# Kernel tuning notes

Hardware: AMD Instinct MI355X
Metric: run time of the kernel (lower is better)

## Reference

```python
import jax, jax.numpy as jnp
import numpy as np

DIM = 768
NUM_BLOCKS = 4
BLOCK = DIM // NUM_BLOCKS
SCALE = 0.02
LAMBDA = 0.01
EPS = 1e-5


def setup_inputs() -> dict:
    key = jax.random.key(0)
    ks = jax.random.split(key, 6)
    B, H, W = 64, 32, 32
    x = jax.random.normal(ks[0], (B, DIM, H, W), dtype=jnp.float32)
    w1 = jax.random.normal(ks[1], (2, NUM_BLOCKS, BLOCK, BLOCK), dtype=jnp.float32) * SCALE
    w2 = jax.random.normal(ks[2], (2, NUM_BLOCKS, BLOCK, BLOCK), dtype=jnp.float32) * SCALE
    b1 = jax.random.normal(ks[3], (2, NUM_BLOCKS, BLOCK), dtype=jnp.float32) * SCALE
    b2 = jax.random.normal(ks[4], (2, NUM_BLOCKS, BLOCK), dtype=jnp.float32) * SCALE
    gamma = jnp.ones((DIM,), dtype=jnp.float32)
    beta = jnp.zeros((DIM,), dtype=jnp.float32)
    return {"x": x, "w1": w1, "w2": w2, "b1": b1, "b2": b2,
            "gamma": gamma, "beta": beta, "H": H, "W": W}


def _softshrink(s, lam):
    return jnp.where(s > lam, s - lam, jnp.where(s < -lam, s + lam, jnp.zeros_like(s)))


def reference(x, w1, w2, b1, b2, gamma, beta, H, W):
    B, C = x.shape[0], x.shape[1]
    nb, bs = NUM_BLOCKS, C // NUM_BLOCKS
    # (B, C, H, W) -> (B, N, C)
    xt = x.reshape(B, C, H * W).transpose(0, 2, 1)
    residual = xt
    # LayerNorm over channel dim
    mu = jnp.mean(xt, axis=-1, keepdims=True)
    var = jnp.mean(jnp.square(xt - mu), axis=-1, keepdims=True)
    xn = (xt - mu) / jnp.sqrt(var + EPS) * gamma + beta
    # (B, N, nb, bs), FFT2 over (N, nb)
    xf = jnp.fft.fft2(xn.reshape(B, H * W, nb, bs), axes=(1, 2), norm='ortho')
    xr, xi = xf.real, xf.imag

    def mul(u, w):
        return jnp.einsum('bnqd,qdk->bnqk', u, w)  # block-diagonal matmul

    r1 = jax.nn.relu(mul(xr, w1[0]) - mul(xi, w1[1]) + b1[0])
    i1 = jax.nn.relu(mul(xr, w1[1]) + mul(xi, w1[0]) + b1[1])
    r2 = mul(r1, w2[0]) - mul(i1, w2[1]) + b2[0]
    i2 = mul(r1, w2[1]) + mul(i1, w2[0]) + b2[1]
    s = jnp.stack([r2, i2], axis=-1)
    s = _softshrink(s, LAMBDA)
    xc = jax.lax.complex(s[..., 0], s[..., 1])
    y = jnp.fft.ifft2(xc, axes=(1, 2), norm='ortho').real  # cast complex->real keeps real part
    y = y.reshape(B, H * W, C) + residual
    return y.transpose(0, 2, 1).reshape(B, C, H, W)
```

## Files before the change

kernel.cpp:

```cpp
#include <hip/hip_runtime.h>
#include <math.h>

#define BB 64
#define CC 768
#define NN 1024
#define BS 192
#define EPS 1e-5f
#define LAM 0.01f

typedef float  f32x4  __attribute__((ext_vector_type(4)));
typedef short  bf16x8 __attribute__((ext_vector_type(8)));

__device__ inline unsigned f2bf(float x) {
    unsigned u = __float_as_uint(x);
    u += 0x7fff + ((u >> 16) & 1);
    return u >> 16;
}
__device__ inline unsigned pack2(float r, float i) { return f2bf(r) | (f2bf(i) << 16); }
__device__ inline float bflo(unsigned v) { return __uint_as_float(v << 16); }
__device__ inline float bfhi(unsigned v) { return __uint_as_float(v & 0xffff0000u); }

__device__ inline int swz(int i) { return i ^ (((i >> 4) & 3) << 2); }

__global__ __launch_bounds__(512) void ln_stats(const float* __restrict__ x,
                                                float* __restrict__ mu,
                                                float* __restrict__ rstd) {
    int tn = threadIdx.x & 63, tc = threadIdx.x >> 6;
    int n = blockIdx.x * 256 + tn * 4, b = blockIdx.y;
    const float* xp = x + (size_t)b * CC * NN + n;
    f32x4 s = (f32x4)0.f, ss = (f32x4)0.f;
    #pragma unroll 4
    for (int c = tc; c < CC; c += 8) {
        f32x4 v = *(const f32x4*)(xp + (size_t)c * NN);
        s += v; ss += v * v;
    }
    __shared__ f32x4 sm[8][64], sq[8][64];
    sm[tc][tn] = s; sq[tc][tn] = ss;
    __syncthreads();
    if (tc == 0) {
        f32x4 S  = sm[0][tn], SS = sq[0][tn];
        #pragma unroll
        for (int i = 1; i < 8; i++) { S += sm[i][tn]; SS += sq[i][tn]; }
        f32x4 m = S * (1.f / 768.f);
        f32x4 r;
        #pragma unroll
        for (int i = 0; i < 4; i++) {
            float var = SS[i] * (1.f / 768.f) - m[i] * m[i];
            r[i] = rsqrtf(var + EPS);
        }
        *(f32x4*)(mu + (size_t)b * NN + n)   = m;
        *(f32x4*)(rstd + (size_t)b * NN + n) = r;
    }
}

__global__ void fwd_fft(const float* __restrict__ x,
                        const float* __restrict__ mu_, const float* __restrict__ rs_,
                        const float* __restrict__ gamma, const float* __restrict__ beta,
                        unsigned* __restrict__ Xp) {
    __shared__ float2 bufs[4][1024];
    int d = blockIdx.x, b = blockIdx.y, tid = threadIdx.x;

    float s1f, c1f;
    __sincosf(-(float)M_PI * 0.5f * (float)tid / 256.f, &s1f, &c1f);
    float c2f = c1f * c1f - s1f * s1f, s2f = 2.f * c1f * s1f;
    float c3f = c2f * c1f - s2f * s1f, s3f = c2f * s1f + s2f * c1f;

    const float* mp = mu_ + b * NN;
    const float* rp = rs_ + b * NN;
    #pragma unroll
    for (int q = 0; q < 4; q++) {
        int c = q * BS + d;
        float g = gamma[c], be = beta[c];
        const float* xp = x + ((size_t)b * CC + c) * NN;
        float v0 = (xp[tid]       - mp[tid])       * rp[tid]       * g + be;
        float v1 = (xp[tid + 256] - mp[tid + 256]) * rp[tid + 256] * g + be;
        float v2 = (xp[tid + 512] - mp[tid + 512]) * rp[tid + 512] * g + be;
        float v3 = (xp[tid + 768] - mp[tid + 768]) * rp[tid + 768] * g + be;
        float t0 = v0 + v2, t1 = v0 - v2, t2 = v1 + v3, t3 = v1 - v3;
        bufs[q][swz(tid)]       = make_float2(t0 + t2, 0.f);
        bufs[q][swz(tid + 256)] = make_float2(t1 * c1f + t3 * s1f, t1 * s1f - t3 * c1f);
        bufs[q][swz(tid + 512)] = make_float2((t0 - t2) * c2f, (t0 - t2) * s2f);
        bufs[q][swz(tid + 768)] = make_float2(t1 * c3f - t3 * s3f, t1 * s3f + t3 * c3f);
    }
    __syncthreads();

    #pragma unroll
    for (int sL = 0; sL < 3; sL++) {
        const int L = 64 >> (2 * sL);
        int j = tid & (L - 1);
        int base = ((tid - j) << 2) + j;
        float s1, c1;
        __sincosf(-(float)M_PI * 0.5f * (float)j / (float)L, &s1, &c1);
        float c2 = c1 * c1 - s1 * s1, s2 = 2.f * c1 * s1;
        float c3 = c2 * c1 - s2 * s1, s3 = c2 * s1 + s2 * c1;
        #pragma unroll
        for (int q = 0; q < 4; q++) {
            float2 a  = bufs[q][swz(base)];
            float2 bb = bufs[q][swz(base + L)];
            float2 cc = bufs[q][swz(base + 2 * L)];
            float2 dd = bufs[q][swz(base + 3 * L)];
            float t0r = a.x + cc.x, t0i = a.y + cc.y;
            float t1r = a.x - cc.x, t1i = a.y - cc.y;
            float t2r = bb.x + dd.x, t2i = bb.y + dd.y;
            float t3r = bb.x - dd.x, t3i = bb.y - dd.y;
            float X0r = t0r + t2r, X0i = t0i + t2i;
            float X2r = t0r - t2r, X2i = t0i - t2i;
            float X1r = t1r + t3i, X1i = t1i - t3r;
            float X3r = t1r - t3i, X3i = t1i + t3r;
            bufs[q][swz(base)]         = make_float2(X0r, X0i);
            bufs[q][swz(base + L)]     = make_float2(X1r * c1 - X1i * s1, X1r * s1 + X1i * c1);
            bufs[q][swz(base + 2 * L)] = make_float2(X2r * c2 - X2i * s2, X2r * s2 + X2i * c2);
            bufs[q][swz(base + 3 * L)] = make_float2(X3r * c3 - X3i * s3, X3r * s3 + X3i * c3);
        }
        __syncthreads();
    }

    float Xr[4][4], Xi[4][4];
    int i0 = swz(4 * tid);
    #pragma unroll
    for (int q = 0; q < 4; q++) {
        const float4* p = (const float4*)&bufs[q][i0];
        float4 u0 = p[0], u1 = p[1];
        float t0r = u0.x + u1.x, t0i = u0.y + u1.y;
        float t1r = u0.x - u1.x, t1i = u0.y - u1.y;
        float t2r = u0.z + u1.z, t2i = u0.w + u1.w;
        float t3r = u0.z - u1.z, t3i = u0.w - u1.w;
        Xr[q][0] = t0r + t2r; Xi[q][0] = t0i + t2i;
        Xr[q][1] = t1r + t3i; Xi[q][1] = t1i - t3r;
        Xr[q][2] = t0r - t2r; Xi[q][2] = t0i - t2i;
        Xr[q][3] = t1r - t3i; Xi[q][3] = t1i + t3r;
    }
    const float sc = 1.f / 64.f;
    unsigned o0[4], o1[4], o2[4], o3[4];
    #pragma unroll
    for (int m = 0; m < 4; m++) {
        float x0r = Xr[0][m], x0i = Xi[0][m];
        float x1r = Xr[1][m], x1i = Xi[1][m];
        float x2r = Xr[2][m], x2i = Xi[2][m];
        float x3r = Xr[3][m], x3i = Xi[3][m];
        float X0r = x0r + x1r + x2r + x3r, X0i = x0i + x1i + x2i + x3i;
        float X2r = x0r - x1r + x2r - x3r, X2i = x0i - x1i + x2i - x3i;
        float X1r = x0r + x1i - x2r - x3i, X1i = x0i - x1r - x2i + x3r;
        float X3r = x0r - x1i - x2r + x3i, X3i = x0i + x1r - x2i - x3r;
        o0[m] = pack2(X0r * sc, X0i * sc);
        o1[m] = pack2(X1r * sc, X1i * sc);
        o2[m] = pack2(X2r * sc, X2i * sc);
        o3[m] = pack2(X3r * sc, X3i * sc);
    }
    size_t qs = (size_t)BS * NN;
    size_t base = (((size_t)b * 4) * BS + d) * NN + 4 * tid;
    *(uint4*)(Xp + base)          = make_uint4(o0[0], o0[1], o0[2], o0[3]);
    *(uint4*)(Xp + base + qs)     = make_uint4(o1[0], o1[1], o1[2], o1[3]);
    *(uint4*)(Xp + base + 2 * qs) = make_uint4(o2[0], o2[1], o2[2], o2[3]);
    *(uint4*)(Xp + base + 3 * qs) = make_uint4(o3[0], o3[1], o3[2], o3[3]);
}

__global__ void pack_b(const float* __restrict__ w, unsigned* __restrict__ Bp) {
    int ch = blockIdx.x, q = blockIdx.y;
    const float* wr = w + (size_t)q * BS * BS;
    const float* wi = w + (size_t)(4 + q) * BS * BS;
    size_t base = ((size_t)q * 12 + ch) * (384 * 16);
    for (int r = 0; r < 24; r++) {
        int idx = r * 256 + threadIdx.x;
        int j = idx >> 4, dd = idx & 15;
        int h = j >> 1;
        int dg = ch * 16 + dd;
        float Wr = wr[(size_t)dg * BS + h];
        float Wi = wi[(size_t)dg * BS + h];
        Bp[base + idx] = (j & 1) ? pack2(Wi, Wr) : pack2(Wr, -Wi);
    }
}

__global__ __launch_bounds__(512, 4) void fused_mlp(const unsigned* __restrict__ Ap,
                                                    const unsigned* __restrict__ Bp1,
                                                    const unsigned* __restrict__ Bp2,
                                                    const float* __restrict__ b1,
                                                    const float* __restrict__ b2,
                                                    unsigned* __restrict__ Yp) {
    __shared__ __align__(16) unsigned tl[12288];

    const int mblk = blockIdx.x;
    const int bq   = blockIdx.y;
    const int q    = bq & 3;
    const int tid  = threadIdx.x;
    const int wave = tid >> 6;
    const int lane = tid & 63;
    const int l15  = lane & 15;
    const int quad = lane >> 4;
    const int jw   = wave * 48;

    const size_t bstride = 384 * 16;
    const unsigned* b1_lane = Bp1 + (size_t)q * 12 * bstride + (jw + l15) * 16 + quad * 4;
    const unsigned* b2_lane = Bp2 + (size_t)q * 12 * bstride + (jw + l15) * 16 + quad * 4;

    {
        const unsigned* abase = Ap + ((size_t)bq * BS) * NN + (size_t)mblk * 64;
        unsigned st[24];
        #pragma unroll
        for (int i = 0; i < 6; i++) {
            int r = (i * 8 + wave) * 4 + quad;
            const unsigned* gp = abase + (size_t)r * NN + l15;
            #pragma unroll
            for (int k = 0; k < 4; k++) st[i * 4 + k] = gp[16 * k];
        }
        #pragma unroll
        for (int i = 0; i < 6; i++) {
            int s = i * 8 + wave;
            unsigned* lp = &tl[s * 256 + quad];
            #pragma unroll
            for (int k = 0; k < 4; k++) lp[(l15 + 16 * k) * 4] = st[i * 4 + k];
        }
    }

    f32x4 acc[3][4];
    #pragma unroll
    for (int i = 0; i < 3; i++)
        #pragma unroll
        for (int j = 0; j < 4; j++)
            acc[i][j] = (f32x4)0.f;

    __syncthreads();

    #pragma unroll
    for (int ch = 0; ch < 12; ch++) {
        const unsigned* tp = &tl[(ch * 4 + quad) * 256];
        const unsigned* bp = b1_lane + ch * bstride;
        bf16x8 af[4], bfr[3];
        #pragma unroll
        for (int tn = 0; tn < 3; tn++) {
            union { uint4 u4; bf16x8 v; } bu;
            bu.u4 = *(const uint4*)(bp + tn * 256);
            bfr[tn] = bu.v;
        }
        #pragma unroll
        for (int tm = 0; tm < 4; tm++)
            af[tm] = *(const bf16x8*)(tp + (tm * 16 + l15) * 4);
        #pragma unroll
        for (int tn = 0; tn < 3; tn++)
            #pragma unroll
            for (int tm = 0; tm < 4; tm++)
                acc[tn][tm] = __builtin_amdgcn_mfma_f32_16x16x32_bf16(bfr[tn], af[tm], acc[tn][tm], 0, 0, 0);
    }

    __syncthreads();

    #pragma unroll
    for (int tn = 0; tn < 3; tn++) {
        int hg = jw >> 1;
        hg += tn * 8 + quad * 2;
        float b0r = b1[q * BS + hg];
        float b0i = b1[768 + q * BS + hg];
        float b1r_ = b1[q * BS + hg + 1];
        float b1i_ = b1[768 + q * BS + hg + 1];
        #pragma unroll
        for (int tm = 0; tm < 4; tm++) {
            int c = tm * 16 + l15;
            f32x4 a = acc[tn][tm];
            float v0 = fmaxf(a[0] + b0r, 0.f);
            float v1 = fmaxf(a[1] + b0i, 0.f);
            float v2 = fmaxf(a[2] + b1r_, 0.f);
            float v3 = fmaxf(a[3] + b1i_, 0.f);
            unsigned* hp = &tl[(hg >> 2) * 256 + c * 4 + (hg & 3)];
            *(uint2*)hp = make_uint2(pack2(v0, v1), pack2(v2, v3));
            acc[tn][tm] = (f32x4)0.f;
        }
    }
    __syncthreads();

    #pragma unroll
    for (int ch = 0; ch < 12; ch++) {
        const unsigned* tp = &tl[(ch * 4 + quad) * 256];
        const unsigned* bp = b2_lane + ch * bstride;
        bf16x8 af[4], bfr[3];
        #pragma unroll
        for (int tn = 0; tn < 3; tn++) {
            union { uint4 u4; bf16x8 v; } bu;
            bu.u4 = *(const uint4*)(bp + tn * 256);
            bfr[tn] = bu.v;
        }
        #pragma unroll
        for (int tm = 0; tm < 4; tm++)
            af[tm] = *(const bf16x8*)(tp + (tm * 16 + l15) * 4);
        #pragma unroll
        for (int tn = 0; tn < 3; tn++)
            #pragma unroll
            for (int tm = 0; tm < 4; tm++)
                acc[tn][tm] = __builtin_amdgcn_mfma_f32_16x16x32_bf16(bfr[tn], af[tm], acc[tn][tm], 0, 0, 0);
    }

    #pragma unroll
    for (int tn = 0; tn < 3; tn++) {
        int hg = (jw >> 1) + tn * 8 + quad * 2;
        float b0r = b2[q * BS + hg];
        float b0i = b2[768 + q * BS + hg];
        float b1r_ = b2[q * BS + hg + 1];
        float b1i_ = b2[768 + q * BS + hg + 1];
        size_t row0 = ((size_t)bq * BS + hg) * NN + (size_t)mblk * 64;
        #pragma unroll
        for (int tm = 0; tm < 4; tm++) {
            int mcol = tm * 16 + l15;
            f32x4 a = acc[tn][tm];
            float v0 = a[0] + b0r, v1 = a[1] + b0i;
            float v2 = a[2] + b1r_, v3 = a[3] + b1i_;
            v0 = (v0 > LAM) ? (v0 - LAM) : ((v0 < -LAM) ? (v0 + LAM) : 0.f);
            v1 = (v1 > LAM) ? (v1 - LAM) : ((v1 < -LAM) ? (v1 + LAM) : 0.f);
            v2 = (v2 > LAM) ? (v2 - LAM) : ((v2 < -LAM) ? (v2 + LAM) : 0.f);
            v3 = (v3 > LAM) ? (v3 - LAM) : ((v3 < -LAM) ? (v3 + LAM) : 0.f);
            Yp[row0 + mcol]      = pack2(v0, v1);
            Yp[row0 + NN + mcol] = pack2(v2, v3);
        }
    }
}

__global__ void inv_fft(const float* __restrict__ x,
                        const unsigned* __restrict__ Yp,
                        float* __restrict__ out) {
    __shared__ float2 bufs[4][1024];
    int d = blockIdx.x, b = blockIdx.y, tid = threadIdx.x;

    float Ar[4][4], Ai[4][4];
    size_t qs = (size_t)BS * NN;
    size_t rowb = (((size_t)b * 4) * BS + d) * NN + 4 * tid;
    #pragma unroll
    for (int q = 0; q < 4; q++) {
        uint4 v = *(const uint4*)(Yp + rowb + (size_t)q * qs);
        Ar[q][0] = bflo(v.x); Ai[q][0] = bfhi(v.x);
        Ar[q][1] = bflo(v.y); Ai[q][1] = bfhi(v.y);
        Ar[q][2] = bflo(v.z); Ai[q][2] = bfhi(v.z);
        Ar[q][3] = bflo(v.w); Ai[q][3] = bfhi(v.w);
    }
    #pragma unroll
    for (int m = 0; m < 4; m++) {
        float x0r = Ar[0][m], x0i = Ai[0][m];
        float x1r = Ar[1][m], x1i = Ai[1][m];
        float x2r = Ar[2][m], x2i = Ai[2][m];
        float x3r = Ar[3][m], x3i = Ai[3][m];
        float Y0r = x0r + x1r + x2r + x3r, Y0i = x0i + x1i + x2i + x3i;
        float Y2r = x0r - x1r + x2r - x3r, Y2i = x0i - x1i + x2i - x3i;
        float Y1r = x0r - x1i - x2r + x3i, Y1i = x0i + x1r - x2i - x3r;
        float Y3r = x0r + x1i - x2r - x3i, Y3i = x0i - x1r - x2i + x3r;
        Ar[0][m] = Y0r; Ai[0][m] = Y0i;
        Ar[1][m] = Y1r; Ai[1][m] = Y1i;
        Ar[2][m] = Y2r; Ai[2][m] = Y2i;
        Ar[3][m] = Y3r; Ai[3][m] = Y3i;
    }
    int i0 = swz(4 * tid);
    #pragma unroll
    for (int q = 0; q < 4; q++) {
        float t0r = Ar[q][0] + Ar[q][2], t0i = Ai[q][0] + Ai[q][2];
        float t1r = Ar[q][0] - Ar[q][2], t1i = Ai[q][0] - Ai[q][2];
        float t2r = Ar[q][1] + Ar[q][3], t2i = Ai[q][1] + Ai[q][3];
        float t3r = Ar[q][1] - Ar[q][3], t3i = Ai[q][1] - Ai[q][3];
        float4* p = (float4*)&bufs[q][i0];
        p[0] = make_float4(t0r + t2r, t0i + t2i, t1r - t3i, t1i + t3r);
        p[1] = make_float4(t0r - t2r, t0i - t2i, t1r + t3i, t1i - t3r);
    }
    __syncthreads();

    #pragma unroll
    for (int sL = 0; sL < 3; sL++) {
        const int L = 4 << (2 * sL);
        int j = tid & (L - 1);
        int base = ((tid - j) << 2) + j;
        float s1, c1;
        __sincosf((float)M_PI * 0.5f * (float)j / (float)L, &s1, &c1);
        float c2 = c1 * c1 - s1 * s1, s2 = 2.f * c1 * s1;
        float c3 = c2 * c1 - s2 * s1, s3 = c2 * s1 + s2 * c1;
        #pragma unroll
        for (int q = 0; q < 4; q++) {
            float2 y0 = bufs[q][swz(base)];
            float2 y1 = bufs[q][swz(base + L)];
            float2 y2 = bufs[q][swz(base + 2 * L)];
            float2 y3 = bufs[q][swz(base + 3 * L)];
            float A1r = y1.x * c1 - y1.y * s1, A1i = y1.x * s1 + y1.y * c1;
            float A2r = y2.x * c2 - y2.y * s2, A2i = y2.x * s2 + y2.y * c2;
            float A3r = y3.x * c3 - y3.y * s3, A3i = y3.x * s3 + y3.y * c3;
            float t0r = y0.x + A2r, t0i = y0.y + A2i;
            float t1r = y0.x - A2r, t1i = y0.y - A2i;
            float t2r = A1r + A3r, t2i = A1i + A3i;
            float t3r = A1r - A3r, t3i = A1i - A3i;
            bufs[q][swz(base)]         = make_float2(t0r + t2r, t0i + t2i);
            bufs[q][swz(base + L)]     = make_float2(t1r - t3i, t1i + t3r);
            bufs[q][swz(base + 2 * L)] = make_float2(t0r - t2r, t0i - t2i);
            bufs[q][swz(base + 3 * L)] = make_float2(t1r + t3i, t1i - t3r);
        }
        __syncthreads();
    }

    float s1f, c1f;
    __sincosf((float)M_PI * 0.5f * (float)tid / 256.f, &s1f, &c1f);
    float c2f = c1f * c1f - s1f * s1f, s2f = 2.f * c1f * s1f;
    float c3f = c2f * c1f - s2f * s1f, s3f = c2f * s1f + s2f * c1f;
    const float sc = 1.f / 64.f;
    #pragma unroll
    for (int q = 0; q < 4; q++) {
        float2 y0 = bufs[q][swz(tid)];
        float2 y1 = bufs[q][swz(tid + 256)];
        float2 y2 = bufs[q][swz(tid + 512)];
        float2 y3 = bufs[q][swz(tid + 768)];
        float A1r = y1.x * c1f - y1.y * s1f, A1i = y1.x * s1f + y1.y * c1f;
        float A2r = y2.x * c2f - y2.y * s2f;
        float A3r = y3.x * c3f - y3.y * s3f, A3i = y3.x * s3f + y3.y * c3f;
        float t0r = y0.x + A2r;
        float t1r = y0.x - A2r;
        float t2r = A1r + A3r;
        float t3i = A1i - A3i;
        size_t row = (((size_t)b * 4 + q) * BS + d) * NN;
        const float* xp = x + row;
        out[row + tid]       = (t0r + t2r) * sc + xp[tid];
        out[row + tid + 256] = (t1r - t3i) * sc + xp[tid + 256];
        out[row + tid + 512] = (t0r - t2r) * sc + xp[tid + 512];
        out[row + tid + 768] = (t1r + t3i) * sc + xp[tid + 768];
    }
}

extern "C" void kernel_launch(void* const* d_in, const int* in_sizes, int n_in,
                              void* d_out, int out_size, void* d_ws, size_t ws_size,
                              hipStream_t stream) {
    const float* x     = (const float*)d_in[0];
    const float* w1    = (const float*)d_in[1];
    const float* w2    = (const float*)d_in[2];
    const float* b1    = (const float*)d_in[3];
    const float* b2    = (const float*)d_in[4];
    const float* gamma = (const float*)d_in[5];
    const float* beta  = (const float*)d_in[6];

    unsigned* Xp = (unsigned*)d_ws;
    float* mu    = (float*)d_ws + (size_t)BB * CC * NN;
    float* rstd  = mu + (size_t)BB * NN;
    unsigned* Bp1 = (unsigned*)(rstd + (size_t)BB * NN);
    unsigned* Bp2 = Bp1 + (size_t)4 * 12 * 384 * 16;
    unsigned* Yp = Xp;

    pack_b<<<dim3(12, 4), 256, 0, stream>>>(w1, Bp1);
    pack_b<<<dim3(12, 4), 256, 0, stream>>>(w2, Bp2);
    ln_stats<<<dim3(NN / 256, BB), 512, 0, stream>>>(x, mu, rstd);
    fwd_fft<<<dim3(BS, BB), 256, 0, stream>>>(x, mu, rstd, gamma, beta, Xp);
    fused_mlp<<<dim3(16, 256), 512, 0, stream>>>(Xp, Bp1, Bp2, b1, b2, Yp);
    inv_fft<<<dim3(BS, BB), 256, 0, stream>>>(x, Yp, (float*)d_out);
}
```

Baseline: 705.8 us.

## Exploit real-input symmetry to halve FFT work in forward and inverse kernels

The forward FFT does the 4-point transform over blocks first and then packs the real-valued channel planes into two complex 1024-point FFTs instead of four. Hermitian symmetry recovers the separate outputs through a conjugate-index permutation (prt). The inverse kernel does the reverse packing, so only two complex inverse FFTs run, and it emits the real output from the combined planes. This halves the shared memory in the forward kernel and the LDS butterfly work, at the cost of extra shuffle passes and syncs. The MLP kernel also drops its occupancy hint and loop unrolling and reorders its fragment loads.

Result: no change. 693.2 us (median of 2 runs) (-1.8%).

```diff
diff --git a/kernel.cpp b/kernel.cpp
--- a/kernel.cpp
+++ b/kernel.cpp
@@ -21,6 +21,16 @@
 __device__ inline float bfhi(unsigned v) { return __uint_as_float(v & 0xffff0000u); }
 
 __device__ inline int swz(int i) { return i ^ (((i >> 4) & 3) << 2); }
+
+__device__ inline int rev4(int p) {
+    return ((p & 3) << 8) | ((p & 12) << 4) | (p & 48) | ((p >> 4) & 12) | ((p >> 8) & 3);
+}
+__device__ inline int prt(int p) {
+    return rev4((1024 - rev4(p)) & 1023);
+}
+__device__ inline float2 cmul(float2 z, float c, float s) {
+    return make_float2(z.x * c - z.y * s, z.x * s + z.y * c);
+}
 
 __global__ __launch_bounds__(512) void ln_stats(const float* __restrict__ x,
                                                 float* __restrict__ mu,
@@ -57,7 +67,7 @@
                         const float* __restrict__ mu_, const float* __restrict__ rs_,
                         const float* __restrict__ gamma, const float* __restrict__ beta,
                         unsigned* __restrict__ Xp) {
-    __shared__ float2 bufs[4][1024];
+    __shared__ float2 bufs[2][1024];
     int d = blockIdx.x, b = blockIdx.y, tid = threadIdx.x;
 
     float s1f, c1f;
@@ -67,20 +77,38 @@
 
     const float* mp = mu_ + b * NN;
     const float* rp = rs_ + b * NN;
+
+    float xv[4][4];
     #pragma unroll
     for (int q = 0; q < 4; q++) {
         int c = q * BS + d;
         float g = gamma[c], be = beta[c];
         const float* xp = x + ((size_t)b * CC + c) * NN;
-        float v0 = (xp[tid]       - mp[tid])       * rp[tid]       * g + be;
-        float v1 = (xp[tid + 256] - mp[tid + 256]) * rp[tid + 256] * g + be;
-        float v2 = (xp[tid + 512] - mp[tid + 512]) * rp[tid + 512] * g + be;
-        float v3 = (xp[tid + 768] - mp[tid + 768]) * rp[tid + 768] * g + be;
-        float t0 = v0 + v2, t1 = v0 - v2, t2 = v1 + v3, t3 = v1 - v3;
-        bufs[q][swz(tid)]       = make_float2(t0 + t2, 0.f);
-        bufs[q][swz(tid + 256)] = make_float2(t1 * c1f + t3 * s1f, t1 * s1f - t3 * c1f);
-        bufs[q][swz(tid + 512)] = make_float2((t0 - t2) * c2f, (t0 - t2) * s2f);
-        bufs[q][swz(tid + 768)] = make_float2(t1 * c3f - t3 * s3f, t1 * s3f + t3 * c3f);
+        #pragma unroll
+        for (int k = 0; k < 4; k++) {
+            int n = tid + 256 * k;
+            xv[q][k] = (xp[n] - mp[n]) * rp[n] * g + be;
+        }
+    }
+    float2 za[4], zb[4];
+    #pragma unroll
+    for (int k = 0; k < 4; k++) {
+        float a = xv[0][k], b1v = xv[1][k], c2v = xv[2][k], d3v = xv[3][k];
+        za[k] = make_float2(a + b1v + c2v + d3v, a - b1v + c2v - d3v);
+        zb[k] = make_float2(a - c2v, d3v - b1v);
+    }
+    #pragma unroll
+    for (int pl = 0; pl < 2; pl++) {
+        float2 z0 = pl ? zb[0] : za[0], z1 = pl ? zb[1] : za[1];
+        float2 z2 = pl ? zb[2] : za[2], z3 = pl ? zb[3] : za[3];
+        float t0r = z0.x + z2.x, t0i = z0.y + z2.y;
+        float t1r = z0.x - z2.x, t1i = z0.y - z2.y;
+        float t2r = z1.x + z3.x, t2i = z1.y + z3.y;
+        float t3r = z1.x - z3.x, t3i = z1.y - z3.y;
+        bufs[pl][swz(tid)] = make_float2(t0r + t2r, t0i + t2i);
+        bufs[pl][swz(tid + 256)] = cmul(make_float2(t1r + t3i, t1i - t3r), c1f, s1f);
+        bufs[pl][swz(tid + 512)] = cmul(make_float2(t0r - t2r, t0i - t2i), c2f, s2f);
+        bufs[pl][swz(tid + 768)] = cmul(make_float2(t1r - t3i, t1i + t3r), c3f, s3f);
     }
     __syncthreads();
 
@@ -94,11 +122,11 @@
         float c2 = c1 * c1 - s1 * s1, s2 = 2.f * c1 * s1;
         float c3 = c2 * c1 - s2 * s1, s3 = c2 * s1 + s2 * c1;
         #pragma unroll
-        for (int q = 0; q < 4; q++) {
-            float2 a  = bufs[q][swz(base)];
-            float2 bb = bufs[q][swz(base + L)];
-            float2 cc = bufs[q][swz(base + 2 * L)];
-            float2 dd = bufs[q][swz(base + 3 * L)];
+        for (int pl = 0; pl < 2; pl++) {
+            float2 a  = bufs[pl][swz(base)];
+            float2 bb = bufs[pl][swz(base + L)];
+            float2 cc = bufs[pl][swz(base + 2 * L)];
+            float2 dd = bufs[pl][swz(base + 3 * L)];
             float t0r = a.x + cc.x, t0i = a.y + cc.y;
             float t1r = a.x - cc.x, t1i = a.y - cc.y;
             float t2r = bb.x + dd.x, t2i = bb.y + dd.y;
@@ -107,45 +135,53 @@
             float X2r = t0r - t2r, X2i = t0i - t2i;
             float X1r = t1r + t3i, X1i = t1i - t3r;
             float X3r = t1r - t3i, X3i = t1i + t3r;
-            bufs[q][swz(base)]         = make_float2(X0r, X0i);
-            bufs[q][swz(base + L)]     = make_float2(X1r * c1 - X1i * s1, X1r * s1 + X1i * c1);
-            bufs[q][swz(base + 2 * L)] = make_float2(X2r * c2 - X2i * s2, X2r * s2 + X2i * c2);
-            bufs[q][swz(base + 3 * L)] = make_float2(X3r * c3 - X3i * s3, X3r * s3 + X3i * c3);
+            bufs[pl][swz(base)]         = make_float2(X0r, X0i);
+            bufs[pl][swz(base + L)]     = make_float2(X1r * c1 - X1i * s1, X1r * s1 + X1i * c1);
+            bufs[pl][swz(base + 2 * L)] = make_float2(X2r * c2 - X2i * s2, X2r * s2 + X2i * c2);
+            bufs[pl][swz(base + 3 * L)] = make_float2(X3r * c3 - X3i * s3, X3r * s3 + X3i * c3);
         }
         __syncthreads();
     }
 
-    float Xr[4][4], Xi[4][4];
     int i0 = swz(4 * tid);
-    #pragma unroll
-    for (int q = 0; q < 4; q++) {
-        const float4* p = (const float4*)&bufs[q][i0];
-        float4 u0 = p[0], u1 = p[1];
-        float t0r = u0.x + u1.x, t0i = u0.y + u1.y;
-        float t1r = u0.x - u1.x, t1i = u0.y - u1.y;
-        float t2r = u0.z + u1.z, t2i = u0.w + u1.w;
-        float t3r = u0.z - u1.z, t3i = u0.w - u1.w;
-        Xr[q][0] = t0r + t2r; Xi[q][0] = t0i + t2i;
-        Xr[q][1] = t1r + t3i; Xi[q][1] = t1i - t3r;
-        Xr[q][2] = t0r - t2r; Xi[q][2] = t0i - t2i;
-        Xr[q][3] = t1r - t3i; Xi[q][3] = t1i + t3r;
-    }
-    const float sc = 1.f / 64.f;
+    float2 A[2][4];
+    #pragma unroll
+    for (int pl = 0; pl < 2; pl++) {
+        const float4* p4 = (const float4*)&bufs[pl][i0];
+        float4 v0 = p4[0], v1 = p4[1];
+        float t0r = v0.x + v1.x, t0i = v0.y + v1.y;
+        float t1r = v0.x - v1.x, t1i = v0.y - v1.y;
+        float t2r = v0.z + v1.z, t2i = v0.w + v1.w;
+        float t3r = v0.z - v1.z, t3i = v0.w - v1.w;
+        A[pl][0] = make_float2(t0r + t2r, t0i + t2i);
+        A[pl][1] = make_float2(t1r + t3i, t1i - t3r);
+        A[pl][2] = make_float2(t0r - t2r, t0i - t2i);
+        A[pl][3] = make_float2(t1r - t3i, t1i + t3r);
+    }
+    #pragma unroll
+    for (int pl = 0; pl < 2; pl++)
+        #pragma unroll
+        for (int j = 0; j < 4; j++)
+            bufs[pl][i0 + j] = A[pl][j];
+    __syncthreads();
+
+    const float sc  = 1.f / 64.f;
+    const float sc2 = 1.f / 128.f;
     unsigned o0[4], o1[4], o2[4], o3[4];
     #pragma unroll
-    for (int m = 0; m < 4; m++) {
-        float x0r = Xr[0][m], x0i = Xi[0][m];
-        float x1r = Xr[1][m], x1i = Xi[1][m];
-        float x2r = Xr[2][m], x2i = Xi[2][m];
-        float x3r = Xr[3][m], x3i = Xi[3][m];
-        float X0r = x0r + x1r + x2r + x3r, X0i = x0i + x1i + x2i + x3i;
-        float X2r = x0r - x1r + x2r - x3r, X2i = x0i - x1i + x2i - x3i;
-        float X1r = x0r + x1i - x2r - x3i, X1i = x0i - x1r - x2i + x3r;
-        float X3r = x0r - x1i - x2r + x3i, X3i = x0i + x1r - x2i - x3r;
-        o0[m] = pack2(X0r * sc, X0i * sc);
-        o1[m] = pack2(X1r * sc, X1i * sc);
-        o2[m] = pack2(X2r * sc, X2i * sc);
-        o3[m] = pack2(X3r * sc, X3i * sc);
+    for (int j = 0; j < 4; j++) {
+        int p = 4 * tid + j;
+        int pq = prt(p);
+        float2 zap = A[0][j], zbp = A[1][j];
+        float2 zaq = bufs[0][swz(pq)];
+        float2 zbq = bufs[1][swz(pq)];
+        float p0r = zap.x + zaq.x, p0i = zap.y - zaq.y;
+        float dr  = zap.x - zaq.x, di  = zap.y + zaq.y;
+        float p2r = di, p2i = -dr;
+        o0[j] = pack2(p0r * sc2, p0i * sc2);
+        o2[j] = pack2(p2r * sc2, p2i * sc2);
+        o1[j] = pack2(zbp.x * sc, zbp.y * sc);
+        o3[j] = pack2(zbq.x * sc, -zbq.y * sc);
     }
     size_t qs = (size_t)BS * NN;
     size_t base = (((size_t)b * 4) * BS + d) * NN + 4 * tid;
@@ -171,12 +207,12 @@
     }
 }
 
-__global__ __launch_bounds__(512, 4) void fused_mlp(const unsigned* __restrict__ Ap,
-                                                    const unsigned* __restrict__ Bp1,
-                                                    const unsigned* __restrict__ Bp2,
-                                                    const float* __restrict__ b1,
-                                                    const float* __restrict__ b2,
-                                                    unsigned* __restrict__ Yp) {
+__global__ __launch_bounds__(512) void fused_mlp(const unsigned* __restrict__ Ap,
+                                                 const unsigned* __restrict__ Bp1,
+                                                 const unsigned* __restrict__ Bp2,
+                                                 const float* __restrict__ b1,
+                                                 const float* __restrict__ b2,
+                                                 unsigned* __restrict__ Yp) {
     __shared__ __align__(16) unsigned tl[12288];
 
     const int mblk = blockIdx.x;
@@ -221,21 +257,20 @@
 
     __syncthreads();
 
-    #pragma unroll
     for (int ch = 0; ch < 12; ch++) {
         const unsigned* tp = &tl[(ch * 4 + quad) * 256];
         const unsigned* bp = b1_lane + ch * bstride;
         bf16x8 af[4], bfr[3];
         #pragma unroll
+        for (int tm = 0; tm < 4; tm++)
+            af[tm] = *(const bf16x8*)(tp + (tm * 16 + l15) * 4);
+        #pragma unroll
         for (int tn = 0; tn < 3; tn++) {
             union { uint4 u4; bf16x8 v; } bu;
             bu.u4 = *(const uint4*)(bp + tn * 256);
             bfr[tn] = bu.v;
         }
         #pragma unroll
-        for (int tm = 0; tm < 4; tm++)
-            af[tm] = *(const bf16x8*)(tp + (tm * 16 + l15) * 4);
-        #pragma unroll
         for (int tn = 0; tn < 3; tn++)
             #pragma unroll
             for (int tm = 0; tm < 4; tm++)
@@ -246,8 +281,7 @@
 
     #pragma unroll
     for (int tn = 0; tn < 3; tn++) {
-        int hg = jw >> 1;
-        hg += tn * 8 + quad * 2;
+        int hg = (jw >> 1) + tn * 8 + quad * 2;
         float b0r = b1[q * BS + hg];
         float b0i = b1[768 + q * BS + hg];
         float b1r_ = b1[q * BS + hg + 1];
@@ -267,20 +301,19 @@
     }
     __syncthreads();
 
-    #pragma unroll
     for (int ch = 0; ch < 12; ch++) {
         const unsigned* tp = &tl[(ch * 4 + quad) * 256];
         const unsigned* bp = b2_lane + ch * bstride;
         bf16x8 af[4], bfr[3];
         #pragma unroll
+        for (int tm = 0; tm < 4; tm++)
+            af[tm] = *(const bf16x8*)(tp + (tm * 16 + l15) * 4);
+        #pragma unroll
         for (int tn = 0; tn < 3; tn++) {
             union { uint4 u4; bf16x8 v; } bu;
             bu.u4 = *(const uint4*)(bp + tn * 256);
             bfr[tn] = bu.v;
         }
-        #pragma unroll
-        for (int tm = 0; tm < 4; tm++)
-            af[tm] = *(const bf16x8*)(tp + (tm * 16 + l15) * 4);
         #pragma unroll
         for (int tn = 0; tn < 3; tn++)
             #pragma unroll
@@ -318,42 +351,52 @@
     __shared__ float2 bufs[4][1024];
     int d = blockIdx.x, b = blockIdx.y, tid = threadIdx.x;
 
-    float Ar[4][4], Ai[4][4];
+    float2 S[4][4];
     size_t qs = (size_t)BS * NN;
     size_t rowb = (((size_t)b * 4) * BS + d) * NN + 4 * tid;
     #pragma unroll
-    for (int q = 0; q < 4; q++) {
-        uint4 v = *(const uint4*)(Yp + rowb + (size_t)q * qs);
-        Ar[q][0] = bflo(v.x); Ai[q][0] = bfhi(v.x);
-        Ar[q][1] = bflo(v.y); Ai[q][1] = bfhi(v.y);
-        Ar[q][2] = bflo(v.z); Ai[q][2] = bfhi(v.z);
-        Ar[q][3] = bflo(v.w); Ai[q][3] = bfhi(v.w);
-    }
-    #pragma unroll
-    for (int m = 0; m < 4; m++) {
-        float x0r = Ar[0][m], x0i = Ai[0][m];
-        float x1r = Ar[1][m], x1i = Ai[1][m];
-        float x2r = Ar[2][m], x2i = Ai[2][m];
-        float x3r = Ar[3][m], x3i = Ai[3][m];
-        float Y0r = x0r + x1r + x2r + x3r, Y0i = x0i + x1i + x2i + x3i;
-        float Y2r = x0r - x1r + x2r - x3r, Y2i = x0i - x1i + x2i - x3i;
-        float Y1r = x0r - x1i - x2r + x3i, Y1i = x0i + x1r - x2i - x3r;
-        float Y3r = x0r + x1i - x2r - x3i, Y3i = x0i - x1r - x2i + x3r;
-        Ar[0][m] = Y0r; Ai[0][m] = Y0i;
-        Ar[1][m] = Y1r; Ai[1][m] = Y1i;
-        Ar[2][m] = Y2r; Ai[2][m] = Y2i;
-        Ar[3][m] = Y3r; Ai[3][m] = Y3i;
+    for (int u = 0; u < 4; u++) {
+        uint4 v = *(const uint4*)(Yp + rowb + (size_t)u * qs);
+        S[u][0] = make_float2(bflo(v.x), bfhi(v.x));
+        S[u][1] = make_float2(bflo(v.y), bfhi(v.y));
+        S[u][2] = make_float2(bflo(v.z), bfhi(v.z));
+        S[u][3] = make_float2(bflo(v.w), bfhi(v.w));
     }
     int i0 = swz(4 * tid);
     #pragma unroll
-    for (int q = 0; q < 4; q++) {
-        float t0r = Ar[q][0] + Ar[q][2], t0i = Ai[q][0] + Ai[q][2];
-        float t1r = Ar[q][0] - Ar[q][2], t1i = Ai[q][0] - Ai[q][2];
-        float t2r = Ar[q][1] + Ar[q][3], t2i = Ai[q][1] + Ai[q][3];
-        float t3r = Ar[q][1] - Ar[q][3], t3i = Ai[q][1] - Ai[q][3];
-        float4* p = (float4*)&bufs[q][i0];
-        p[0] = make_float4(t0r + t2r, t0i + t2i, t1r - t3i, t1i + t3r);
-        p[1] = make_float4(t0r - t2r, t0i - t2i, t1r + t3i, t1i - t3r);
+    for (int u = 0; u < 4; u++)
+        #pragma unroll
+        for (int j = 0; j < 4; j++)
+            bufs[u][i0 + j] = S[u][j];
+    __syncthreads();
+
+    float2 Wa[4], Wb[4];
+    #pragma unroll
+    for (int j = 0; j < 4; j++) {
+        int p = 4 * tid + j;
+        int pq = prt(p);
+        float2 s0q = bufs[0][swz(pq)];
+        float2 s2q = bufs[2][swz(pq)];
+        float2 s3q = bufs[3][swz(pq)];
+        float h0r = S[0][j].x + s0q.x, h0i = S[0][j].y - s0q.y;
+        float h2r = S[2][j].x + s2q.x, h2i = S[2][j].y - s2q.y;
+        Wa[j] = make_float2(h0r - h2i, h0i + h2r);
+        Wb[j] = make_float2(S[1][j].x + s3q.x, S[1][j].y - s3q.y);
+    }
+    __syncthreads();
+
+    #pragma unroll
+    for (int pl = 0; pl < 2; pl++) {
+        float2 w0 = pl ? Wb[0] : Wa[0], w1 = pl ? Wb[1] : Wa[1];
+        float2 w2 = pl ? Wb[2] : Wa[2], w3 = pl ? Wb[3] : Wa[3];
+        float t0r = w0.x + w2.x, t0i = w0.y + w2.y;
+        float t1r = w0.x - w2.x, t1i = w0.y - w2.y;
+        float t2r = w1.x + w3.x, t2i = w1.y + w3.y;
+        float t3r = w1.x - w3.x, t3i = w1.y - w3.y;
+        bufs[pl][i0 + 0] = make_float2(t0r + t2r, t0i + t2i);
+        bufs[pl][i0 + 1] = make_float2(t1r - t3i, t1i + t3r);
+        bufs[pl][i0 + 2] = make_float2(t0r - t2r, t0i - t2i);
+        bufs[pl][i0 + 3] = make_float2(t1r + t3i, t1i - t3r);
     }
     __syncthreads();
 
@@ -367,11 +410,11 @@
         float c2 = c1 * c1 - s1 * s1, s2 = 2.f * c1 * s1;
         float c3 = c2 * c1 - s2 * s1, s3 = c2 * s1 + s2 * c1;
         #pragma unroll
-        for (int q = 0; q < 4; q++) {
-            float2 y0 = bufs[q][swz(base)];
-            float2 y1 = bufs[q][swz(base + L)];
-            float2 y2 = bufs[q][swz(base + 2 * L)];
-            float2 y3 = bufs[q][swz(base + 3 * L)];
+        for (int pl = 0; pl < 2; pl++) {
+            float2 y0 = bufs[pl][swz(base)];
+            float2 y1 = bufs[pl][swz(base + L)];
+            float2 y2 = bufs[pl][swz(base + 2 * L)];
+            float2 y3 = bufs[pl][swz(base + 3 * L)];
             float A1r = y1.x * c1 - y1.y * s1, A1i = y1.x * s1 + y1.y * c1;
             float A2r = y2.x * c2 - y2.y * s2, A2i = y2.x * s2 + y2.y * c2;
             float A3r = y3.x * c3 - y3.y * s3, A3i = y3.x * s3 + y3.y * c3;
@@ -379,10 +422,10 @@
             float t1r = y0.x - A2r, t1i = y0.y - A2i;
             float t2r = A1r + A3r, t2i = A1i + A3i;
             float t3r = A1r - A3r, t3i = A1i - A3i;
-            bufs[q][swz(base)]         = make_float2(t0r + t2r, t0i + t2i);
-            bufs[q][swz(base + L)]     = make_float2(t1r - t3i, t1i + t3r);
-            bufs[q][swz(base + 2 * L)] = make_float2(t0r - t2r, t0i - t2i);
-            bufs[q][swz(base + 3 * L)] = make_float2(t1r + t3i, t1i - t3r);
+            bufs[pl][swz(base)]         = make_float2(t0r + t2r, t0i + t2i);
+            bufs[pl][swz(base + L)]     = make_float2(t1r - t3i, t1i + t3r);
+            bufs[pl][swz(base + 2 * L)] = make_float2(t0r - t2r, t0i - t2i);
+            bufs[pl][swz(base + 3 * L)] = make_float2(t1r + t3i, t1i - t3r);
         }
         __syncthreads();
     }
@@ -391,26 +434,42 @@
     __sincosf((float)M_PI * 0.5f * (float)tid / 256.f, &s1f, &c1f);
     float c2f = c1f * c1f - s1f * s1f, s2f = 2.f * c1f * s1f;
     float c3f = c2f * c1f - s2f * s1f, s3f = c2f * s1f + s2f * c1f;
-    const float sc = 1.f / 64.f;
-    #pragma unroll
-    for (int q = 0; q < 4; q++) {
-        float2 y0 = bufs[q][swz(tid)];
-        float2 y1 = bufs[q][swz(tid + 256)];
-        float2 y2 = bufs[q][swz(tid + 512)];
-        float2 y3 = bufs[q][swz(tid + 768)];
-        float A1r = y1.x * c1f - y1.y * s1f, A1i = y1.x * s1f + y1.y * c1f;
-        float A2r = y2.x * c2f - y2.y * s2f;
-        float A3r = y3.x * c3f - y3.y * s3f, A3i = y3.x * s3f + y3.y * c3f;
-        float t0r = y0.x + A2r;
-        float t1r = y0.x - A2r;
-        float t2r = A1r + A3r;
-        float t3i = A1i - A3i;
-        size_t row = (((size_t)b * 4 + q) * BS + d) * NN;
-        const float* xp = x + row;
-        out[row + tid]       = (t0r + t2r) * sc + xp[tid];
-        out[row + tid + 256] = (t1r - t3i) * sc + xp[tid + 256];
-        out[row + tid + 512] = (t0r - t2r) * sc + xp[tid + 512];
-        out[row + tid + 768] = (t1r + t3i) * sc + xp[tid + 768];
+
+    float2 Va[4], Vb[4];
+    #pragma unroll
+    for (int pl = 0; pl < 2; pl++) {
+        float2 y0 = bufs[pl][swz(tid)];
+        float2 y1 = bufs[pl][swz(tid + 256)];
+        float2 y2 = bufs[pl][swz(tid + 512)];
+        float2 y3 = bufs[pl][swz(tid + 768)];
+        float2 A1 = cmul(y1, c1f, s1f);
+        float2 A2 = cmul(y2, c2f, s2f);
+        float2 A3 = cmul(y3, c3f, s3f);
+        float t0r = y0.x + A2.x, t0i = y0.y + A2.y;
+        float t1r = y0.x - A2.x, t1i = y0.y - A2.y;
+        float t2r = A1.x + A3.x, t2i = A1.y + A3.y;
+        float t3r = A1.x - A3.x, t3i = A1.y - A3.y;
+        float2* V = pl ? Vb : Va;
+        V[0] = make_float2(t0r + t2r, t0i + t2i);
+        V[1] = make_float2(t1r - t3i, t1i + t3r);
+        V[2] = make_float2(t0r - t2r, t0i - t2i);
+        V[3] = make_float2(t1r + t3i, t1i - t3r);
+    }
+
+    const float sc = 1.f / 128.f;
+    size_t row0 = (((size_t)b * 4 + 0) * BS + d) * NN;
+    size_t row1 = (((size_t)b * 4 + 1) * BS + d) * NN;
+    size_t row2 = (((size_t)b * 4 + 2) * BS + d) * NN;
+    size_t row3 = (((size_t)b * 4 + 3) * BS + d) * NN;
+    #pragma unroll
+    for (int k = 0; k < 4; k++) {
+        int n = tid + 256 * k;
+        float V0 = Va[k].x, V2 = Va[k].y;
+        float R1 = Vb[k].x, I1 = Vb[k].y;
+        out[row0 + n] = (V0 + V2 + 2.f * R1) * sc + x[row0 + n];
+        out[row1 + n] = (V0 - V2 - 2.f * I1) * sc + x[row1 + n];
+        out[row2 + n] = (V0 + V2 - 2.f * R1) * sc + x[row2 + n];
+        out[row3 + n] = (V0 - V2 + 2.f * I1) * sc + x[row3 + n];
     }
 }
 
```
